# Performance work log

Hardware: AMD Instinct MI355X
Metric: run time of the kernel (lower is better)

## Reference

```python
import jax, jax.numpy as jnp
import numpy as np


def setup_inputs() -> dict:
    key = jax.random.key(0)
    qkv = jax.random.normal(key, (8, 1536, 2048), dtype=jnp.float32)
    return {"qkv": qkv, "n_heads": 8}


def reference(qkv, n_heads):
    # qkv: [N, H*3*C, T] -> output [N, H*C, T]
    bs, width, length = qkv.shape
    assert width % (3 * n_heads) == 0
    ch = width // (3 * n_heads)
    qkv_r = qkv.reshape(bs * n_heads, 3 * ch, length)
    q, k, v = qkv_r[:, :ch], qkv_r[:, ch:2 * ch], qkv_r[:, 2 * ch:]
    scale = 1.0 / np.sqrt(np.sqrt(ch))  # applied to both q and k
    # [B, T, S] scores
    weight = jnp.einsum('bct,bcs->bts', q * scale, k * scale)
    weight = jax.nn.softmax(weight.astype(jnp.float32), axis=-1).astype(weight.dtype)
    a = jnp.einsum('bts,bcs->bct', weight, v)
    return a.reshape(bs, n_heads * ch, length)
```

## Files before the change

### kernel.cpp

```cpp
#include <hip/hip_runtime.h>


typedef __bf16 bf16;
typedef __bf16 bf16x4 __attribute__((ext_vector_type(4)));
typedef __bf16 bf16x8 __attribute__((ext_vector_type(8)));
typedef float  f32x4  __attribute__((ext_vector_type(4)));
typedef float  f32x16 __attribute__((ext_vector_type(16)));
typedef unsigned int u32;

#define NLEN 2048
#define DCH  64
#define HSTR (NLEN * DCH * 2)
#define WS_K (16u * 1024u * 1024u)
#define WS_V (32u * 1024u * 1024u)
#define WS_NEED (48u * 1024u * 1024u)
#define PSCALE 0.42466119f

__device__ __forceinline__ int swzK(int row, int cb) {
    return row * 128 + ((((cb >> 4) ^ row) & 7) << 4) + (cb & 15);
}
__device__ __forceinline__ int swzO(int row, int cb) {
    int g = cb >> 4;
    g = (g & ~7) | ((g ^ row) & 7);
    return row * 512 + (g << 4) + (cb & 15);
}

__device__ __forceinline__ void gload16(const char* g, char* l) {
    __builtin_amdgcn_global_load_lds((const __attribute__((address_space(1))) void*)g,
                                     (__attribute__((address_space(3))) void*)l, 16, 0, 0);
}

__global__ __launch_bounds__(256)
void prep(const float* __restrict__ qkv, char* __restrict__ ws)
{
    const int tid  = threadIdx.x;
    const int pb   = blockIdx.x;
    const int head = blockIdx.y;
    const int type = blockIdx.z;

    const float* src = qkv + (size_t)head * (3 * DCH) * NLEN + (size_t)type * DCH * NLEN;
    char* dst = ws + (type == 0 ? 0u : (type == 1 ? WS_K : WS_V))
                   + (size_t)head * HSTR + (size_t)pb * 8192;

    if (type < 2) {
        __shared__ float T[64][65];
        #pragma unroll
        for (int p = 0; p < 4; ++p) {
            int idx = tid + p * 256;
            int c = idx >> 4, q4 = idx & 15;
            float4 f = *(const float4*)(src + (size_t)c * NLEN + pb * 64 + q4 * 4);
            T[q4 * 4 + 0][c] = f.x * PSCALE;
            T[q4 * 4 + 1][c] = f.y * PSCALE;
            T[q4 * 4 + 2][c] = f.z * PSCALE;
            T[q4 * 4 + 3][c] = f.w * PSCALE;
        }
        __syncthreads();
        #pragma unroll
        for (int p = 0; p < 2; ++p) {
            int gidx = tid + p * 256;
            int s = gidx >> 3, G = gidx & 7;
            if (type == 0) {
                int c0 = (G ^ (s & 7)) * 8;
                bf16 tmp[8];
                #pragma unroll
                for (int j = 0; j < 8; ++j) tmp[j] = (bf16)T[s][c0 + j];
                *(bf16x8*)(dst + s * 128 + G * 16) = *(bf16x8*)tmp;
            } else {
                const int kc = G >> 1, hi = G & 1;
                bf16 tmp[8];
                #pragma unroll
                for (int j = 0; j < 8; ++j) tmp[j] = (bf16)T[s][G * 8 + j];
                *(bf16x8*)(dst + kc * 2048 + ((s >> 5) & 1) * 1024 + hi * 512
                               + (s & 31) * 16) = *(bf16x8*)tmp;
            }
        }
    } else {
        const int c = tid >> 2, m = tid & 3;
        const float* sp = src + (size_t)c * NLEN + pb * 64 + m * 16;
        float f[16];
        #pragma unroll
        for (int j = 0; j < 4; ++j) *(f32x4*)(f + 4 * j) = *(const f32x4*)(sp + 4 * j);
        #pragma unroll
        for (int gl = 0; gl < 2; ++gl) {
            bf16 tmp[8];
            #pragma unroll
            for (int j = 0; j < 8; ++j) tmp[j] = (bf16)f[gl * 8 + j];
            *(bf16x8*)(dst + m * 2048 + ((c >> 5) & 1) * 1024 + gl * 512
                           + (c & 31) * 16) = *(bf16x8*)tmp;
        }
    }
}

__device__ __forceinline__ void expcvt(f32x16& slo, f32x16& shi, float& l, bf16x8 pa[4])
{
    float a = 0.f, b = 0.f, c = 0.f, d = 0.f;
    #pragma unroll
    for (int r = 0; r < 16; r += 4) {
        slo[r+0] = __builtin_amdgcn_exp2f(slo[r+0]); a += slo[r+0];
        slo[r+1] = __builtin_amdgcn_exp2f(slo[r+1]); b += slo[r+1];
        slo[r+2] = __builtin_amdgcn_exp2f(slo[r+2]); c += slo[r+2];
        slo[r+3] = __builtin_amdgcn_exp2f(slo[r+3]); d += slo[r+3];
    }
    #pragma unroll
    for (int r = 0; r < 16; r += 4) {
        shi[r+0] = __builtin_amdgcn_exp2f(shi[r+0]); a += shi[r+0];
        shi[r+1] = __builtin_amdgcn_exp2f(shi[r+1]); b += shi[r+1];
        shi[r+2] = __builtin_amdgcn_exp2f(shi[r+2]); c += shi[r+2];
        shi[r+3] = __builtin_amdgcn_exp2f(shi[r+3]); d += shi[r+3];
    }
    l += (a + b) + (c + d);
    #pragma unroll
    for (int ks = 0; ks < 4; ++ks) {
        const f32x16& pp = (ks < 2) ? slo : shi;
        const int rb = (ks & 1) * 8;
        u32 X, X2, Y, Y2;
        asm("v_cvt_pk_bf16_f32 %0, %1, %2" : "=v"(X)  : "v"(pp[rb + 0]), "v"(pp[rb + 1]));
        asm("v_cvt_pk_bf16_f32 %0, %1, %2" : "=v"(X2) : "v"(pp[rb + 2]), "v"(pp[rb + 3]));
        asm("v_cvt_pk_bf16_f32 %0, %1, %2" : "=v"(Y)  : "v"(pp[rb + 4]), "v"(pp[rb + 5]));
        asm("v_cvt_pk_bf16_f32 %0, %1, %2" : "=v"(Y2) : "v"(pp[rb + 6]), "v"(pp[rb + 7]));
        asm("v_permlane32_swap_b32 %0, %1" : "+v"(X),  "+v"(Y));
        asm("v_permlane32_swap_b32 %0, %1" : "+v"(X2), "+v"(Y2));
        u32 wds[4] = {X, X2, Y, Y2};
        pa[ks] = *(bf16x8*)wds;
    }
}

__global__ __launch_bounds__(128, 2)
void attn_main(const char* __restrict__ ws, float* __restrict__ out)
{
    const int tid  = threadIdx.x;
    const int lane = tid & 63;
    const int w    = tid >> 6;
    const int hi   = lane >> 5;
    const int ll5  = lane & 31;

    const int bid  = blockIdx.x;
    const int j    = bid >> 3;
    const int head = (bid & 7) * 8 + (j & 7);
    const int tblk = j >> 3;
    const int t0   = tblk * 128;

    const char* Qb = ws + (size_t)head * HSTR + (size_t)t0 * 128;
    const char* Kb = ws + WS_K + (size_t)head * HSTR;
    const char* Vb = ws + WS_V + (size_t)head * HSTR;

    __shared__ __align__(16) char lds[32768];

    #pragma unroll
    for (int i = 0; i < 8; ++i)
        gload16(Qb + tid * 16 + i * 2048, lds + tid * 16 + i * 2048);
    asm volatile("s_waitcnt vmcnt(0)");
    __syncthreads();

    bf16x8 qf0[4], qf1[4];
    #pragma unroll
    for (int kc = 0; kc < 4; ++kc) {
        qf0[kc] = *(const bf16x8*)(lds + swzK(w * 64 + ll5,      kc * 32 + hi * 16));
        qf1[kc] = *(const bf16x8*)(lds + swzK(w * 64 + 32 + ll5, kc * 32 + hi * 16));
    }

    const int voff = hi * 512 + ll5 * 16;

    bf16x8 kf0[4], kf1[4];
    #pragma unroll
    for (int kc = 0; kc < 4; ++kc) {
        kf0[kc] = *(const bf16x8*)(Kb + voff + kc * 2048);
        kf1[kc] = *(const bf16x8*)(Kb + voff + kc * 2048 + 1024);
    }

    f32x16 o00 = {}, o01 = {}, o10 = {}, o11 = {};
    float l0 = 0.f, l1 = 0.f;

    #pragma unroll 1
    for (int i = 0; i < 32; ++i) {
        bf16x8 vf0[4], vf1[4];
        {
            const char* Vt = Vb + (size_t)i * 8192 + voff;
            #pragma unroll
            for (int ks = 0; ks < 4; ++ks) {
                vf0[ks] = *(const bf16x8*)(Vt + ks * 2048);
                vf1[ks] = *(const bf16x8*)(Vt + ks * 2048 + 1024);
            }
        }

        f32x16 sa = {}, sb = {};
        #pragma unroll
        for (int kc = 0; kc < 4; ++kc) {
            sa = __builtin_amdgcn_mfma_f32_32x32x16_bf16(kf0[kc], qf0[kc], sa, 0, 0, 0);
            sb = __builtin_amdgcn_mfma_f32_32x32x16_bf16(kf1[kc], qf0[kc], sb, 0, 0, 0);
        }
        bf16x8 pa0[4];
        expcvt(sa, sb, l0, pa0);

        f32x16 sc = {}, sd = {};
        #pragma unroll
        for (int kc = 0; kc < 4; ++kc) {
            sc = __builtin_amdgcn_mfma_f32_32x32x16_bf16(kf0[kc], qf1[kc], sc, 0, 0, 0);
            sd = __builtin_amdgcn_mfma_f32_32x32x16_bf16(kf1[kc], qf1[kc], sd, 0, 0, 0);
        }

        if (i != 31) {
            const char* Kt = Kb + (size_t)(i + 1) * 8192 + voff;
            #pragma unroll
            for (int kc = 0; kc < 4; ++kc) {
                kf0[kc] = *(const bf16x8*)(Kt + kc * 2048);
                kf1[kc] = *(const bf16x8*)(Kt + kc * 2048 + 1024);
            }
        }

        bf16x8 pa1[4];
        expcvt(sc, sd, l1, pa1);

        #pragma unroll
        for (int ks = 0; ks < 4; ++ks) {
            o00 = __builtin_amdgcn_mfma_f32_32x32x16_bf16(pa0[ks], vf0[ks], o00, 0, 0, 0);
            o01 = __builtin_amdgcn_mfma_f32_32x32x16_bf16(pa0[ks], vf1[ks], o01, 0, 0, 0);
            o10 = __builtin_amdgcn_mfma_f32_32x32x16_bf16(pa1[ks], vf0[ks], o10, 0, 0, 0);
            o11 = __builtin_amdgcn_mfma_f32_32x32x16_bf16(pa1[ks], vf1[ks], o11, 0, 0, 0);
        }
    }

    const float lf0 = l0 + __shfl_xor(l0, 32);
    const float lf1 = l1 + __shfl_xor(l1, 32);
    const float li0 = 1.0f / lf0;
    const float li1 = 1.0f / lf1;
    float a0[16], a1[16];
    #pragma unroll
    for (int r = 0; r < 16; ++r) {
        const int src = (r & 3) + 8 * (r >> 2) + 4 * hi;
        a0[r] = __shfl(li0, src);
        a1[r] = __shfl(li1, src);
    }
    #pragma unroll
    for (int r = 0; r < 16; ++r) {
        o00[r] *= a0[r]; o01[r] *= a0[r];
        o10[r] *= a1[r]; o11[r] *= a1[r];
    }

    __syncthreads();
    float* Of = (float*)lds;
    #pragma unroll
    for (int th = 0; th < 2; ++th) {
        const f32x16& v0 = th ? o10 : o00;
        const f32x16& v1 = th ? o11 : o01;
        #pragma unroll
        for (int jj = 0; jj < 4; ++jj) {
            const int tb = w * 64 + th * 32 + 8 * jj + 4 * hi;
            f32x4 u0, u1;
            #pragma unroll
            for (int r = 0; r < 4; ++r) { u0[r] = v0[4 * jj + r]; u1[r] = v1[4 * jj + r]; }
            *(f32x4*)((char*)Of + swzO(ll5,      tb * 4)) = u0;
            *(f32x4*)((char*)Of + swzO(32 + ll5, tb * 4)) = u1;
        }
    }
    __syncthreads();

    float* op = out + (size_t)head * DCH * NLEN + t0;
    #pragma unroll
    for (int ch = 0; ch < 16; ++ch) {
        const int idx = tid + ch * 128;
        const int c = idx >> 5, tq = idx & 31;
        f32x4 v = *(const f32x4*)((char*)Of + swzO(c, tq * 16));
        *(float4*)(op + (size_t)c * NLEN + tq * 4) = *(float4*)&v;
    }
}

#define QSCALE_FB 0.35355339059327373f
__global__ __launch_bounds__(512, 2)
void attn_fwd(const float* __restrict__ qkv, float* __restrict__ out)
{
    const int tid  = threadIdx.x;
    const int lane = tid & 63;
    const int w    = tid >> 6;
    const int lg   = lane >> 4;
    const int ll   = lane & 15;
    const int tblk = blockIdx.x;
    const int head = blockIdx.y;
    const int t0   = tblk * 128;

    const float* qp = qkv + (size_t)head * (3 * DCH) * NLEN;
    const float* kp = qp + (size_t)DCH * NLEN;
    const float* vp = kp + (size_t)DCH * NLEN;

    __shared__ __align__(16) char lds[48 * 1024];
    char* Qs = lds;
    char* Ks = lds + 16 * 1024;
    char* Vs = lds + 24 * 1024;
    char* Ps = lds + 32 * 1024 + w * 2048;

    {
        const int G = tid >> 6;
        #pragma unroll
        for (int it = 0; it < 2; ++it) {
            const int t = (tid & 63) + it * 64;
            const float* src = qp + (size_t)(G * 8) * NLEN + t0 + t;
            bf16 tmp[8];
            #pragma unroll
            for (int j = 0; j < 8; ++j) tmp[j] = (bf16)(src[(size_t)j * NLEN] * QSCALE_FB);
            *(bf16x8*)(Qs + swzK(t, G * 16)) = *(bf16x8*)tmp;
        }
    }
    __syncthreads();
    bf16x8 qf[2];
    #pragma unroll
    for (int kk = 0; kk < 2; ++kk)
        qf[kk] = *(const bf16x8*)(Qs + swzK(w * 16 + ll, kk * 64 + lg * 16));

    f32x4 o[4] = {};
    float m_r = -3.0e38f, l_r = 0.f;

    for (int sb = 0; sb < NLEN / 64; ++sb) {
        const int s0 = sb * 64;
        __syncthreads();
        {
            const int s = tid & 63, G = tid >> 6;
            const float* src = kp + (size_t)(G * 8) * NLEN + s0 + s;
            bf16 tmp[8];
            #pragma unroll
            for (int j = 0; j < 8; ++j) tmp[j] = (bf16)(src[(size_t)j * NLEN] * QSCALE_FB);
            *(bf16x8*)(Ks + swzK(s, G * 16)) = *(bf16x8*)tmp;
        }
        {
            const int c = tid >> 3, s8 = tid & 7;
            const float* src = vp + (size_t)c * NLEN + s0 + s8 * 8;
            const float4 f0 = *(const float4*)src;
            const float4 f1 = *(const float4*)(src + 4);
            bf16 tmp[8] = {(bf16)f0.x, (bf16)f0.y, (bf16)f0.z, (bf16)f0.w,
                           (bf16)f1.x, (bf16)f1.y, (bf16)f1.z, (bf16)f1.w};
            *(bf16x8*)(Vs + swzK(c, s8 * 16)) = *(bf16x8*)tmp;
        }
        __syncthreads();

        f32x4 sf[4] = {};
        #pragma unroll
        for (int kk = 0; kk < 2; ++kk)
            #pragma unroll
            for (int fs = 0; fs < 4; ++fs) {
                bf16x8 a = *(const bf16x8*)(Ks + swzK(fs * 16 + ll, kk * 64 + lg * 16));
                sf[fs] = __builtin_amdgcn_mfma_f32_16x16x32_bf16(a, qf[kk], sf[fs], 0, 0, 0);
            }

        float mx;
        {
            f32x4 m4 = sf[0];
            #pragma unroll
            for (int fs = 1; fs < 4; ++fs) {
                m4[0] = fmaxf(m4[0], sf[fs][0]); m4[1] = fmaxf(m4[1], sf[fs][1]);
                m4[2] = fmaxf(m4[2], sf[fs][2]); m4[3] = fmaxf(m4[3], sf[fs][3]);
            }
            mx = fmaxf(fmaxf(m4[0], m4[1]), fmaxf(m4[2], m4[3]));
        }
        mx = fmaxf(mx, __shfl_xor(mx, 16));
        mx = fmaxf(mx, __shfl_xor(mx, 32));
        const float mnew = fmaxf(m_r, mx);
        const float corr = exp2f((m_r - mnew) * 1.4426950408889634f);
        m_r = mnew;
        const float cm = mnew * 1.4426950408889634f;

        float psum = 0.f;
        #pragma unroll
        for (int fs = 0; fs < 4; ++fs) {
            bf16x4 pw;
            #pragma unroll
            for (int r = 0; r < 4; ++r) {
                float p = exp2f(fmaf(sf[fs][r], 1.4426950408889634f, -cm));
                psum += p;
                pw[r] = (bf16)p;
            }
            *(bf16x4*)(Ps + swzK(ll, 32 * fs + 8 * lg)) = pw;
        }
        psum += __shfl_xor(psum, 16);
        psum += __shfl_xor(psum, 32);
        l_r = l_r * corr + psum;

        float corr4[4];
        #pragma unroll
        for (int r = 0; r < 4; ++r) corr4[r] = __shfl(corr, 4 * lg + r);
        #pragma unroll
        for (int cf = 0; cf < 4; ++cf)
            #pragma unroll
            for (int r = 0; r < 4; ++r) o[cf][r] *= corr4[r];

        #pragma unroll
        for (int kk = 0; kk < 2; ++kk) {
            bf16x8 pa = *(const bf16x8*)(Ps + swzK(ll, kk * 64 + lg * 16));
            #pragma unroll
            for (int cf = 0; cf < 4; ++cf) {
                bf16x8 b = *(const bf16x8*)(Vs + swzK(cf * 16 + ll, kk * 64 + lg * 16));
                o[cf] = __builtin_amdgcn_mfma_f32_16x16x32_bf16(pa, b, o[cf], 0, 0, 0);
            }
        }
    }

    __syncthreads();
    const float linv = 1.0f / l_r;
    float linv4[4];
    #pragma unroll
    for (int r = 0; r < 4; ++r) linv4[r] = __shfl(linv, 4 * lg + r);
    float* Of = (float*)lds;
    #pragma unroll
    for (int cf = 0; cf < 4; ++cf) {
        f32x4 ov;
        #pragma unroll
        for (int r = 0; r < 4; ++r) ov[r] = o[cf][r] * linv4[r];
        *(f32x4*)((char*)Of + swzO(cf * 16 + ll, (w * 16 + 4 * lg) * 4)) = ov;
    }
    __syncthreads();
    float* op = out + (size_t)head * DCH * NLEN + t0;
    #pragma unroll
    for (int it = 0; it < 4; ++it) {
        const int idx = tid + it * 512;
        const int c = idx >> 5, tq = idx & 31;
        f32x4 v = *(const f32x4*)((char*)Of + swzO(c, tq * 16));
        *(float4*)(op + (size_t)c * NLEN + tq * 4) = *(float4*)&v;
    }
}

extern "C" void kernel_launch(void* const* d_in, const int* in_sizes, int n_in,
                              void* d_out, int out_size, void* d_ws, size_t ws_size,
                              hipStream_t stream)
{
    const float* qkv = (const float*)d_in[0];
    float* out = (float*)d_out;
    if (ws_size >= (size_t)WS_NEED) {
        char* ws = (char*)d_ws;
        prep<<<dim3(32, 64, 3), 256, 0, stream>>>(qkv, ws);
        attn_main<<<dim3(1024), 128, 0, stream>>>(ws, out);
    } else {
        attn_fwd<<<dim3(16, 64), 512, 0, stream>>>(qkv, out);
    }
}
```

Baseline: 100.8 us.

## Split query tile across four waves with one 32-row tile each

Each block now runs 256 threads (4 waves), and each wave owns 32 query rows instead of 64. The register-resident K prefetch is removed; K and V fragments are loaded directly from global memory inside the loop. The aim is to cut per-wave register use so that more waves fit per CU (launch bounds 256,4), trading explicit software prefetching for latency hiding through occupancy. Each K/V tile is now reused by only one 32-row query tile per wave, so global/L2 traffic per unit of compute roughly doubles.

```diff
diff --git a/kernel.cpp b/kernel.cpp
--- a/kernel.cpp
+++ b/kernel.cpp
@@ -125,7 +125,7 @@
     }
 }
 
-__global__ __launch_bounds__(128, 2)
+__global__ __launch_bounds__(256, 4)
 void attn_main(const char* __restrict__ ws, float* __restrict__ out)
 {
     const int tid  = threadIdx.x;
@@ -147,118 +147,73 @@
     __shared__ __align__(16) char lds[32768];
 
     #pragma unroll
-    for (int i = 0; i < 8; ++i)
-        gload16(Qb + tid * 16 + i * 2048, lds + tid * 16 + i * 2048);
+    for (int i = 0; i < 4; ++i)
+        gload16(Qb + tid * 16 + i * 4096, lds + tid * 16 + i * 4096);
     asm volatile("s_waitcnt vmcnt(0)");
     __syncthreads();
 
-    bf16x8 qf0[4], qf1[4];
-    #pragma unroll
-    for (int kc = 0; kc < 4; ++kc) {
-        qf0[kc] = *(const bf16x8*)(lds + swzK(w * 64 + ll5,      kc * 32 + hi * 16));
-        qf1[kc] = *(const bf16x8*)(lds + swzK(w * 64 + 32 + ll5, kc * 32 + hi * 16));
-    }
+    bf16x8 qf[4];
+    #pragma unroll
+    for (int kc = 0; kc < 4; ++kc)
+        qf[kc] = *(const bf16x8*)(lds + swzK(w * 32 + ll5, kc * 32 + hi * 16));
 
     const int voff = hi * 512 + ll5 * 16;
 
-    bf16x8 kf0[4], kf1[4];
-    #pragma unroll
-    for (int kc = 0; kc < 4; ++kc) {
-        kf0[kc] = *(const bf16x8*)(Kb + voff + kc * 2048);
-        kf1[kc] = *(const bf16x8*)(Kb + voff + kc * 2048 + 1024);
-    }
-
-    f32x16 o00 = {}, o01 = {}, o10 = {}, o11 = {};
-    float l0 = 0.f, l1 = 0.f;
+    f32x16 o0 = {}, o1 = {};
+    float l_r = 0.f;
 
     #pragma unroll 1
     for (int i = 0; i < 32; ++i) {
-        bf16x8 vf0[4], vf1[4];
-        {
-            const char* Vt = Vb + (size_t)i * 8192 + voff;
-            #pragma unroll
-            for (int ks = 0; ks < 4; ++ks) {
-                vf0[ks] = *(const bf16x8*)(Vt + ks * 2048);
-                vf1[ks] = *(const bf16x8*)(Vt + ks * 2048 + 1024);
-            }
-        }
+        const char* Kt = Kb + (size_t)i * 8192 + voff;
+        const char* Vt = Vb + (size_t)i * 8192 + voff;
 
         f32x16 sa = {}, sb = {};
         #pragma unroll
         for (int kc = 0; kc < 4; ++kc) {
-            sa = __builtin_amdgcn_mfma_f32_32x32x16_bf16(kf0[kc], qf0[kc], sa, 0, 0, 0);
-            sb = __builtin_amdgcn_mfma_f32_32x32x16_bf16(kf1[kc], qf0[kc], sb, 0, 0, 0);
-        }
-        bf16x8 pa0[4];
-        expcvt(sa, sb, l0, pa0);
-
-        f32x16 sc = {}, sd = {};
-        #pragma unroll
-        for (int kc = 0; kc < 4; ++kc) {
-            sc = __builtin_amdgcn_mfma_f32_32x32x16_bf16(kf0[kc], qf1[kc], sc, 0, 0, 0);
-            sd = __builtin_amdgcn_mfma_f32_32x32x16_bf16(kf1[kc], qf1[kc], sd, 0, 0, 0);
-        }
-
-        if (i != 31) {
-            const char* Kt = Kb + (size_t)(i + 1) * 8192 + voff;
-            #pragma unroll
-            for (int kc = 0; kc < 4; ++kc) {
-                kf0[kc] = *(const bf16x8*)(Kt + kc * 2048);
-                kf1[kc] = *(const bf16x8*)(Kt + kc * 2048 + 1024);
-            }
-        }
-
-        bf16x8 pa1[4];
-        expcvt(sc, sd, l1, pa1);
+            bf16x8 k0 = *(const bf16x8*)(Kt + kc * 2048);
+            bf16x8 k1 = *(const bf16x8*)(Kt + kc * 2048 + 1024);
+            sa = __builtin_amdgcn_mfma_f32_32x32x16_bf16(k0, qf[kc], sa, 0, 0, 0);
+            sb = __builtin_amdgcn_mfma_f32_32x32x16_bf16(k1, qf[kc], sb, 0, 0, 0);
+        }
+
+        bf16x8 pa[4];
+        expcvt(sa, sb, l_r, pa);
 
         #pragma unroll
         for (int ks = 0; ks < 4; ++ks) {
-            o00 = __builtin_amdgcn_mfma_f32_32x32x16_bf16(pa0[ks], vf0[ks], o00, 0, 0, 0);
-            o01 = __builtin_amdgcn_mfma_f32_32x32x16_bf16(pa0[ks], vf1[ks], o01, 0, 0, 0);
-            o10 = __builtin_amdgcn_mfma_f32_32x32x16_bf16(pa1[ks], vf0[ks], o10, 0, 0, 0);
-            o11 = __builtin_amdgcn_mfma_f32_32x32x16_bf16(pa1[ks], vf1[ks], o11, 0, 0, 0);
-        }
-    }
-
-    const float lf0 = l0 + __shfl_xor(l0, 32);
-    const float lf1 = l1 + __shfl_xor(l1, 32);
-    const float li0 = 1.0f / lf0;
-    const float li1 = 1.0f / lf1;
-    float a0[16], a1[16];
-    #pragma unroll
-    for (int r = 0; r < 16; ++r) {
-        const int src = (r & 3) + 8 * (r >> 2) + 4 * hi;
-        a0[r] = __shfl(li0, src);
-        a1[r] = __shfl(li1, src);
-    }
-    #pragma unroll
-    for (int r = 0; r < 16; ++r) {
-        o00[r] *= a0[r]; o01[r] *= a0[r];
-        o10[r] *= a1[r]; o11[r] *= a1[r];
-    }
+            bf16x8 b0 = *(const bf16x8*)(Vt + ks * 2048);
+            bf16x8 b1 = *(const bf16x8*)(Vt + ks * 2048 + 1024);
+            o0 = __builtin_amdgcn_mfma_f32_32x32x16_bf16(pa[ks], b0, o0, 0, 0, 0);
+            o1 = __builtin_amdgcn_mfma_f32_32x32x16_bf16(pa[ks], b1, o1, 0, 0, 0);
+        }
+    }
+
+    const float lf = l_r + __shfl_xor(l_r, 32);
+    const float linv = 1.0f / lf;
+    float li[16];
+    #pragma unroll
+    for (int r = 0; r < 16; ++r)
+        li[r] = __shfl(linv, (r & 3) + 8 * (r >> 2) + 4 * hi);
+    #pragma unroll
+    for (int r = 0; r < 16; ++r) { o0[r] *= li[r]; o1[r] *= li[r]; }
 
     __syncthreads();
     float* Of = (float*)lds;
     #pragma unroll
-    for (int th = 0; th < 2; ++th) {
-        const f32x16& v0 = th ? o10 : o00;
-        const f32x16& v1 = th ? o11 : o01;
-        #pragma unroll
-        for (int jj = 0; jj < 4; ++jj) {
-            const int tb = w * 64 + th * 32 + 8 * jj + 4 * hi;
-            f32x4 u0, u1;
-            #pragma unroll
-            for (int r = 0; r < 4; ++r) { u0[r] = v0[4 * jj + r]; u1[r] = v1[4 * jj + r]; }
-            *(f32x4*)((char*)Of + swzO(ll5,      tb * 4)) = u0;
-            *(f32x4*)((char*)Of + swzO(32 + ll5, tb * 4)) = u1;
-        }
+    for (int jj = 0; jj < 4; ++jj) {
+        const int tb = w * 32 + 8 * jj + 4 * hi;
+        f32x4 u0, u1;
+        #pragma unroll
+        for (int r = 0; r < 4; ++r) { u0[r] = o0[4 * jj + r]; u1[r] = o1[4 * jj + r]; }
+        *(f32x4*)((char*)Of + swzO(ll5,      tb * 4)) = u0;
+        *(f32x4*)((char*)Of + swzO(32 + ll5, tb * 4)) = u1;
     }
     __syncthreads();
 
     float* op = out + (size_t)head * DCH * NLEN + t0;
     #pragma unroll
-    for (int ch = 0; ch < 16; ++ch) {
-        const int idx = tid + ch * 128;
+    for (int ch = 0; ch < 8; ++ch) {
+        const int idx = tid + ch * 256;
         const int c = idx >> 5, tq = idx & 31;
         f32x4 v = *(const f32x4*)((char*)Of + swzO(c, tq * 16));
         *(float4*)(op + (size_t)c * NLEN + tq * 4) = *(float4*)&v;
@@ -425,7 +380,7 @@
     if (ws_size >= (size_t)WS_NEED) {
         char* ws = (char*)d_ws;
         prep<<<dim3(32, 64, 3), 256, 0, stream>>>(qkv, ws);
-        attn_main<<<dim3(1024), 128, 0, stream>>>(ws, out);
+        attn_main<<<dim3(1024), 256, 0, stream>>>(ws, out);
     } else {
         attn_fwd<<<dim3(16, 64), 512, 0, stream>>>(qkv, out);
     }
```

Result: slower. 113.3 us (+12.4%).

## Drop LDS staging for Q and output, load V just-in-time, swap PV operands

Applied to the files above, without the earlier changes.

Q is now stored unswizzled and read directly from global memory into registers instead of being staged through LDS. V fragments are loaded right before each PV MFMA rather than up front, and the MFMA operand order is swapped so the output accumulator comes out transposed. Each lane can then write its normalized results straight to global memory, which removes the LDS round trip, the barriers and the cross-lane shuffles for the normalization factors. The tradeoffs are scalar, less coalesced output stores and V load latency that is now exposed right next to the MFMAs.

```diff
diff --git a/kernel.cpp b/kernel.cpp
--- a/kernel.cpp
+++ b/kernel.cpp
@@ -23,11 +23,6 @@
     int g = cb >> 4;
     g = (g & ~7) | ((g ^ row) & 7);
     return row * 512 + (g << 4) + (cb & 15);
-}
-
-__device__ __forceinline__ void gload16(const char* g, char* l) {
-    __builtin_amdgcn_global_load_lds((const __attribute__((address_space(1))) void*)g,
-                                     (__attribute__((address_space(3))) void*)l, 16, 0, 0);
 }
 
 __global__ __launch_bounds__(256)
@@ -60,10 +55,9 @@
             int gidx = tid + p * 256;
             int s = gidx >> 3, G = gidx & 7;
             if (type == 0) {
-                int c0 = (G ^ (s & 7)) * 8;
                 bf16 tmp[8];
                 #pragma unroll
-                for (int j = 0; j < 8; ++j) tmp[j] = (bf16)T[s][c0 + j];
+                for (int j = 0; j < 8; ++j) tmp[j] = (bf16)T[s][G * 8 + j];
                 *(bf16x8*)(dst + s * 128 + G * 16) = *(bf16x8*)tmp;
             } else {
                 const int kc = G >> 1, hi = G & 1;
@@ -144,19 +138,11 @@
     const char* Kb = ws + WS_K + (size_t)head * HSTR;
     const char* Vb = ws + WS_V + (size_t)head * HSTR;
 
-    __shared__ __align__(16) char lds[32768];
-
-    #pragma unroll
-    for (int i = 0; i < 8; ++i)
-        gload16(Qb + tid * 16 + i * 2048, lds + tid * 16 + i * 2048);
-    asm volatile("s_waitcnt vmcnt(0)");
-    __syncthreads();
-
     bf16x8 qf0[4], qf1[4];
     #pragma unroll
     for (int kc = 0; kc < 4; ++kc) {
-        qf0[kc] = *(const bf16x8*)(lds + swzK(w * 64 + ll5,      kc * 32 + hi * 16));
-        qf1[kc] = *(const bf16x8*)(lds + swzK(w * 64 + 32 + ll5, kc * 32 + hi * 16));
+        qf0[kc] = *(const bf16x8*)(Qb + (size_t)(w * 64 + ll5) * 128      + kc * 32 + hi * 16);
+        qf1[kc] = *(const bf16x8*)(Qb + (size_t)(w * 64 + 32 + ll5) * 128 + kc * 32 + hi * 16);
     }
 
     const int voff = hi * 512 + ll5 * 16;
@@ -173,15 +159,7 @@
 
     #pragma unroll 1
     for (int i = 0; i < 32; ++i) {
-        bf16x8 vf0[4], vf1[4];
-        {
-            const char* Vt = Vb + (size_t)i * 8192 + voff;
-            #pragma unroll
-            for (int ks = 0; ks < 4; ++ks) {
-                vf0[ks] = *(const bf16x8*)(Vt + ks * 2048);
-                vf1[ks] = *(const bf16x8*)(Vt + ks * 2048 + 1024);
-            }
-        }
+        const char* Vt = Vb + (size_t)i * 8192 + voff;
 
         f32x16 sa = {}, sb = {};
         #pragma unroll
@@ -213,55 +191,26 @@
 
         #pragma unroll
         for (int ks = 0; ks < 4; ++ks) {
-            o00 = __builtin_amdgcn_mfma_f32_32x32x16_bf16(pa0[ks], vf0[ks], o00, 0, 0, 0);
-            o01 = __builtin_amdgcn_mfma_f32_32x32x16_bf16(pa0[ks], vf1[ks], o01, 0, 0, 0);
-            o10 = __builtin_amdgcn_mfma_f32_32x32x16_bf16(pa1[ks], vf0[ks], o10, 0, 0, 0);
-            o11 = __builtin_amdgcn_mfma_f32_32x32x16_bf16(pa1[ks], vf1[ks], o11, 0, 0, 0);
-        }
-    }
-
-    const float lf0 = l0 + __shfl_xor(l0, 32);
-    const float lf1 = l1 + __shfl_xor(l1, 32);
-    const float li0 = 1.0f / lf0;
-    const float li1 = 1.0f / lf1;
-    float a0[16], a1[16];
+            bf16x8 a0 = *(const bf16x8*)(Vt + ks * 2048);
+            bf16x8 a1 = *(const bf16x8*)(Vt + ks * 2048 + 1024);
+            o00 = __builtin_amdgcn_mfma_f32_32x32x16_bf16(a0, pa0[ks], o00, 0, 0, 0);
+            o01 = __builtin_amdgcn_mfma_f32_32x32x16_bf16(a1, pa0[ks], o01, 0, 0, 0);
+            o10 = __builtin_amdgcn_mfma_f32_32x32x16_bf16(a0, pa1[ks], o10, 0, 0, 0);
+            o11 = __builtin_amdgcn_mfma_f32_32x32x16_bf16(a1, pa1[ks], o11, 0, 0, 0);
+        }
+    }
+
+    const float li0 = 1.0f / (l0 + __shfl_xor(l0, 32));
+    const float li1 = 1.0f / (l1 + __shfl_xor(l1, 32));
+
+    float* opt = out + (size_t)head * DCH * NLEN + t0 + w * 64 + ll5;
     #pragma unroll
     for (int r = 0; r < 16; ++r) {
-        const int src = (r & 3) + 8 * (r >> 2) + 4 * hi;
-        a0[r] = __shfl(li0, src);
-        a1[r] = __shfl(li1, src);
-    }
-    #pragma unroll
-    for (int r = 0; r < 16; ++r) {
-        o00[r] *= a0[r]; o01[r] *= a0[r];
-        o10[r] *= a1[r]; o11[r] *= a1[r];
-    }
-
-    __syncthreads();
-    float* Of = (float*)lds;
-    #pragma unroll
-    for (int th = 0; th < 2; ++th) {
-        const f32x16& v0 = th ? o10 : o00;
-        const f32x16& v1 = th ? o11 : o01;
-        #pragma unroll
-        for (int jj = 0; jj < 4; ++jj) {
-            const int tb = w * 64 + th * 32 + 8 * jj + 4 * hi;
-            f32x4 u0, u1;
-            #pragma unroll
-            for (int r = 0; r < 4; ++r) { u0[r] = v0[4 * jj + r]; u1[r] = v1[4 * jj + r]; }
-            *(f32x4*)((char*)Of + swzO(ll5,      tb * 4)) = u0;
-            *(f32x4*)((char*)Of + swzO(32 + ll5, tb * 4)) = u1;
-        }
-    }
-    __syncthreads();
-
-    float* op = out + (size_t)head * DCH * NLEN + t0;
-    #pragma unroll
-    for (int ch = 0; ch < 16; ++ch) {
-        const int idx = tid + ch * 128;
-        const int c = idx >> 5, tq = idx & 31;
-        f32x4 v = *(const f32x4*)((char*)Of + swzO(c, tq * 16));
-        *(float4*)(op + (size_t)c * NLEN + tq * 4) = *(float4*)&v;
+        const int c = (r & 3) + 8 * (r >> 2) + 4 * hi;
+        opt[(size_t)c * NLEN]             = o00[r] * li0;
+        opt[(size_t)(32 + c) * NLEN]      = o01[r] * li0;
+        opt[(size_t)c * NLEN + 32]        = o10[r] * li1;
+        opt[(size_t)(32 + c) * NLEN + 32] = o11[r] * li1;
     }
 }
 
```

New measurement: 99.87 us. Within noise of the previous version (-0.9%).
